# Kernel optimization log

Hardware: AMD Instinct MI355X
Metric: run time of the kernel (lower is better)

Reference implementation:

```python
import jax, jax.numpy as jnp
import numpy as np

N, E = 50000, 800000
NFEAT, NHID, NHEADS, NCLASS = 512, 64, 8, 64
ALPHA = 0.2  # leaky relu negative slope


def setup_inputs() -> dict:
    key = jax.random.key(0)
    ks = jax.random.split(key, 8)
    x = jax.random.normal(ks[0], (N, NFEAT), jnp.float32)
    row = jax.random.randint(ks[1], (E,), 0, N)  # destination node i of each edge
    col = jax.random.randint(ks[2], (E,), 0, N)  # source node j of each edge
    W = jax.random.normal(ks[3], (NHEADS, NFEAT, NHID), jnp.float32) * (1.0 / np.sqrt(NFEAT))
    a = jax.random.normal(ks[4], (NHEADS, 2 * NHID), jnp.float32) * 0.1
    W_out = jax.random.normal(ks[5], (NHID * NHEADS, NCLASS), jnp.float32) * (1.0 / np.sqrt(NHID * NHEADS))
    a_out = jax.random.normal(ks[6], (2 * NCLASS,), jnp.float32) * 0.1
    return {"x": x, "row": row, "col": col, "W": W, "a": a, "W_out": W_out, "a_out": a_out}


def _gat_layer(h, W, a, row, col, n, alpha, concat):
    # h: [N, F_in], W: [F_in, F'], a: [2*F']
    Wh = h @ W                                   # [N, F']
    f = Wh.shape[-1]
    f_dst = Wh @ a[:f]                           # a^T part for target node i, [N]
    f_src = Wh @ a[f:]                           # a^T part for source node j, [N]
    e = jax.nn.leaky_relu(f_dst[row] + f_src[col], alpha)       # [E] attention logits
    # numerically stable segment softmax over incoming edges of each node
    m = jax.ops.segment_max(e, row, num_segments=n)
    m = jnp.where(jnp.isneginf(m), 0.0, m)       # nodes with no in-edges
    p = jnp.exp(e - m[row])
    denom = jax.ops.segment_sum(p, row, num_segments=n)
    att = p / jnp.maximum(denom[row], 1e-16)     # [E]
    out = jax.ops.segment_sum(att[:, None] * Wh[col], row, num_segments=n)  # [N, F']
    return jax.nn.elu(out) if concat else out


def reference(x, row, col, W, a, W_out, a_out):
    # eval mode: F.dropout is a no-op
    heads = [_gat_layer(x, W[h], a[h], row, col, N, ALPHA, True) for h in range(NHEADS)]
    h = jnp.concatenate(heads, axis=1)           # [N, NHID*NHEADS]
    return _gat_layer(h, W_out, a_out, row, col, N, ALPHA, False)  # [N, NCLASS]
```

## Files before the change

kernel.cpp:

```cpp
#include <hip/hip_runtime.h>
#include <cstdint>
#include <cstddef>

#define NN      50000
#define MPAD    50048
#define EE      800000
#define NHEADS  8
#define HID_TOT 512
#define NCLASS  64
#define ALPHA_LRELU 0.2f
#define NB1     196

typedef unsigned short u16;
typedef __attribute__((ext_vector_type(8))) unsigned short ushort8;
typedef __attribute__((ext_vector_type(4))) unsigned short ushort4v;

__device__ __forceinline__ float bf2f(u16 v) {
    return __uint_as_float(((unsigned)v) << 16);
}
__device__ __forceinline__ u16 f2bf(float f) {
    unsigned u = __float_as_uint(f);
    return (u16)((u + 0x7fffu + ((u >> 16) & 1u)) >> 16);
}

#define PREP_R0 (MPAD * 64)
#define PREP_R1 (512 * 512)
#define PREP_R2 (64 * 512)
#define PREP_R3 (NN / 4)
#define PREP_TOT (PREP_R0 + PREP_R1 + PREP_R2 + PREP_R3)

__global__ __launch_bounds__(256) void prep_all(const float* __restrict__ x,
                                                const float* __restrict__ W,
                                                const float* __restrict__ W_out,
                                                u16* __restrict__ xb,
                                                u16* __restrict__ Wt1,
                                                u16* __restrict__ Wto,
                                                int* __restrict__ cnt) {
    int g = blockIdx.x * 256 + threadIdx.x;
    if (g < PREP_R0) {
        int r = g >> 6;
        int c = (g & 63) * 8;
        ushort8 o = (ushort8)0;
        if (r < NN) {
            const float4 v0 = *(const float4*)(x + (size_t)r * 512 + c);
            const float4 v1 = *(const float4*)(x + (size_t)r * 512 + c + 4);
            o[0] = f2bf(v0.x); o[1] = f2bf(v0.y); o[2] = f2bf(v0.z); o[3] = f2bf(v0.w);
            o[4] = f2bf(v1.x); o[5] = f2bf(v1.y); o[6] = f2bf(v1.z); o[7] = f2bf(v1.w);
        }
        *(ushort8*)(xb + (size_t)r * 512 + c) = o;
        return;
    }
    g -= PREP_R0;
    if (g < PREP_R1) {
        int c = g >> 9, f = g & 511;
        int h = c >> 6, j = c & 63;
        Wt1[g] = f2bf(W[(h << 15) + (f << 6) + j]);
        return;
    }
    g -= PREP_R1;
    if (g < PREP_R2) {
        int n = g >> 9, k = g & 511;
        Wto[g] = f2bf(W_out[k * 64 + n]);
        return;
    }
    g -= PREP_R2;
    if (g < PREP_R3) {
        *(int4*)(cnt + g * 4) = make_int4(0, 0, 0, 0);
    }
}


__global__ void hist_rows(const int* __restrict__ row, int* __restrict__ cnt) {
    int e = blockIdx.x * 256 + threadIdx.x;
    if (e >= EE) return;
    atomicAdd(&cnt[row[e]], 1);
}

__global__ __launch_bounds__(256) void scan_blocksum(const int* __restrict__ cnt,
                                                     int* __restrict__ bsum) {
    int idx = blockIdx.x * 256 + threadIdx.x;
    int v = (idx < NN) ? cnt[idx] : 0;
    #pragma unroll
    for (int o = 32; o; o >>= 1) v += __shfl_xor(v, o);
    __shared__ int sw[4];
    int wave = threadIdx.x >> 6;
    if ((threadIdx.x & 63) == 0) sw[wave] = v;
    __syncthreads();
    if (threadIdx.x == 0) bsum[blockIdx.x] = sw[0] + sw[1] + sw[2] + sw[3];
}

__global__ __launch_bounds__(256) void scan_bsums(const int* __restrict__ bsum,
                                                  int* __restrict__ boff) {
    __shared__ int sh[256];
    int t = threadIdx.x;
    int v = (t < NB1) ? bsum[t] : 0;
    sh[t] = v;
    __syncthreads();
    for (int o = 1; o < 256; o <<= 1) {
        int cur = sh[t];
        int add = (t >= o) ? sh[t - o] : 0;
        __syncthreads();
        sh[t] = cur + add;
        __syncthreads();
    }
    if (t < NB1) boff[t] = sh[t] - v;
}

__global__ __launch_bounds__(256) void scan_write(const int* __restrict__ cnt,
                                                  const int* __restrict__ boff,
                                                  int* __restrict__ start,
                                                  int* __restrict__ wr) {
    __shared__ int sh[256];
    int t = threadIdx.x;
    int idx = blockIdx.x * 256 + t;
    int c = (idx < NN) ? cnt[idx] : 0;
    sh[t] = c;
    __syncthreads();
    for (int o = 1; o < 256; o <<= 1) {
        int cur = sh[t];
        int add = (t >= o) ? sh[t - o] : 0;
        __syncthreads();
        sh[t] = cur + add;
        __syncthreads();
    }
    if (idx < NN) {
        int excl = boff[blockIdx.x] + sh[t] - c;
        start[idx] = excl;
        wr[idx] = excl;
    }
    if (idx == 0) start[NN] = EE;
}

__global__ void scatter_edges(const int* __restrict__ row, const int* __restrict__ col,
                              int* __restrict__ wr, int* __restrict__ ecol) {
    int e = blockIdx.x * 256 + threadIdx.x;
    if (e >= EE) return;
    int i = row[e];
    int pos = atomicAdd(&wr[i], 1);
    ecol[pos] = col[e];
}


__device__ __forceinline__ void load_lds_128(const u16* g, u16* l) {
    __builtin_amdgcn_global_load_lds((const __attribute__((address_space(1))) void*)g,
                                     (__attribute__((address_space(3))) void*)l,
                                     16, 0, 0);
}

typedef __attribute__((ext_vector_type(8))) short frag8;
typedef __attribute__((ext_vector_type(4))) float f32x4;

template <int BN, int OUT_MODE, int FUSE>
__global__ __launch_bounds__(256) void gemm_bf16(const u16* __restrict__ A,
                                                 const u16* __restrict__ Bt,
                                                 void* __restrict__ Cv,
                                                 int M, int N, int K,
                                                 const float* __restrict__ av,
                                                 float* __restrict__ fd,
                                                 float* __restrict__ fs) {
    constexpr int BM = 128, BK = 32;
    constexpr int WN = BN / 2;
    constexpr int NT = WN / 16;
    __shared__ u16 As[BM * BK];
    __shared__ u16 Bs[BN * BK];
    __shared__ float pd[2][2][64];
    __shared__ float ps[2][2][64];
    const int tid = threadIdx.x;
    const int wave = tid >> 6, lane = tid & 63;
    const int wm = wave & 1, wn = wave >> 1;
    const int bm = blockIdx.x * BM, bn = blockIdx.y * BN;
    const int q = lane >> 4, lr = lane & 15;

    f32x4 acc[4][NT] = {};

    for (int k0 = 0; k0 < K; k0 += BK) {
        #pragma unroll
        for (int c = wave; c < (BM * BK) / 512; c += 4) {
            int f = c * 512 + lane * 8;
            int row = f >> 5, ck = f & 31;
            load_lds_128(A + (size_t)(bm + row) * K + k0 + ck, As + c * 512);
        }
        #pragma unroll
        for (int c = wave; c < (BN * BK) / 512; c += 4) {
            int f = c * 512 + lane * 8;
            int row = f >> 5, ck = f & 31;
            load_lds_128(Bt + (size_t)(bn + row) * K + k0 + ck, Bs + c * 512);
        }
        __syncthreads();
        frag8 af[4], bfr[NT];
        #pragma unroll
        for (int am = 0; am < 4; am++)
            af[am] = *(const frag8*)(As + (wm * 64 + am * 16 + lr) * 32 + q * 8);
        #pragma unroll
        for (int bt = 0; bt < NT; bt++)
            bfr[bt] = *(const frag8*)(Bs + (wn * WN + bt * 16 + lr) * 32 + q * 8);
        #pragma unroll
        for (int am = 0; am < 4; am++)
            #pragma unroll
            for (int bt = 0; bt < NT; bt++)
                acc[am][bt] = __builtin_amdgcn_mfma_f32_16x16x32_bf16(af[am], bfr[bt], acc[am][bt], 0, 0, 0);
        __syncthreads();
    }

    float adv[NT], adv2[NT];
    int hd = 0;
    if (FUSE == 1) {
        hd = blockIdx.y * 2 + wn;
        const float* ah = av + hd * 128;
        #pragma unroll
        for (int bt = 0; bt < NT; bt++) {
            adv[bt]  = ah[bt * 16 + lr];
            adv2[bt] = ah[64 + bt * 16 + lr];
        }
    }
    if (FUSE == 2) {
        #pragma unroll
        for (int bt = 0; bt < NT; bt++) {
            adv[bt]  = av[wn * WN + bt * 16 + lr];
            adv2[bt] = av[64 + wn * WN + bt * 16 + lr];
        }
    }

    #pragma unroll
    for (int am = 0; am < 4; am++) {
        #pragma unroll
        for (int reg = 0; reg < 4; reg++) {
            int gr = bm + wm * 64 + am * 16 + q * 4 + reg;
            bool inb = gr < M;
            if (inb) {
                #pragma unroll
                for (int bt = 0; bt < NT; bt++) {
                    int gc = bn + wn * WN + bt * 16 + lr;
                    float v = acc[am][bt][reg];
                    if (OUT_MODE == 0) ((float*)Cv)[(size_t)gr * N + gc] = v;
                    else               ((u16*)Cv)[(size_t)gr * N + gc] = f2bf(v);
                }
            }
            if (FUSE != 0) {
                float sd = 0.f, ss = 0.f;
                #pragma unroll
                for (int bt = 0; bt < NT; bt++) {
                    float v = acc[am][bt][reg];
                    sd += v * adv[bt];
                    ss += v * adv2[bt];
                }
                #pragma unroll
                for (int o = 1; o < 16; o <<= 1) {
                    sd += __shfl_xor(sd, o);
                    ss += __shfl_xor(ss, o);
                }
                if (FUSE == 1) {
                    if (lr == 0 && inb) {
                        fd[gr * 8 + hd] = sd;
                        fs[gr * 8 + hd] = ss;
                    }
                } else {
                    if (lr == 0) {
                        int rr = am * 16 + q * 4 + reg;
                        pd[wm][wn][rr] = sd;
                        ps[wm][wn][rr] = ss;
                    }
                }
            }
        }
    }
    if (FUSE == 2) {
        __syncthreads();
        if (tid < 128) {
            int wmm = tid >> 6, rr = tid & 63;
            int gr = bm + wmm * 64 + rr;
            if (gr < M) {
                fd[gr] = pd[wmm][0][rr] + pd[wmm][1][rr];
                fs[gr] = ps[wmm][0][rr] + ps[wmm][1][rr];
            }
        }
    }
}

__global__ __launch_bounds__(256) void agg1_fused(const int* __restrict__ start,
                                                  const int* __restrict__ ecol,
                                                  const float* __restrict__ fd,
                                                  const float* __restrict__ fs,
                                                  const u16* __restrict__ Whb,
                                                  u16* __restrict__ h1b) {
    const int i = blockIdx.x * 4 + (threadIdx.x >> 6);
    const int lane = threadIdx.x & 63;
    const int hh = lane >> 3;
    const int st = start[i], en = start[i + 1];
    const float fdv = fd[i * 8 + hh];

    float acc[8] = {};
    float den = 0.f;
    int t = st;
    for (; t + 2 <= en; t += 2) {
        int j0 = ecol[t], j1 = ecol[t + 1];
        float v0 = fdv + fs[j0 * 8 + hh]; v0 = v0 > 0.f ? v0 : ALPHA_LRELU * v0;
        float v1 = fdv + fs[j1 * 8 + hh]; v1 = v1 > 0.f ? v1 : ALPHA_LRELU * v1;
        float p0 = __expf(v0);
        float p1 = __expf(v1);
        ushort8 w0 = *(const ushort8*)(Whb + (size_t)j0 * HID_TOT + lane * 8);
        ushort8 w1 = *(const ushort8*)(Whb + (size_t)j1 * HID_TOT + lane * 8);
        den += p0 + p1;
        #pragma unroll
        for (int k = 0; k < 8; k++) acc[k] += p0 * bf2f(w0[k]);
        #pragma unroll
        for (int k = 0; k < 8; k++) acc[k] += p1 * bf2f(w1[k]);
    }
    if (t < en) {
        int j = ecol[t];
        float v = fdv + fs[j * 8 + hh]; v = v > 0.f ? v : ALPHA_LRELU * v;
        float p = __expf(v);
        den += p;
        ushort8 wv = *(const ushort8*)(Whb + (size_t)j * HID_TOT + lane * 8);
        #pragma unroll
        for (int k = 0; k < 8; k++) acc[k] += p * bf2f(wv[k]);
    }
    float rden = 1.0f / fmaxf(den, 1e-16f);
    ushort8 o8;
    #pragma unroll
    for (int k = 0; k < 8; k++) {
        float v = acc[k] * rden;
        v = v > 0.f ? v : (__expf(v) - 1.0f);
        o8[k] = f2bf(v);
    }
    *(ushort8*)(h1b + (size_t)i * HID_TOT + lane * 8) = o8;
}

__global__ __launch_bounds__(256) void agg2_fused(const int* __restrict__ start,
                                                  const int* __restrict__ ecol,
                                                  const float* __restrict__ fd,
                                                  const float* __restrict__ fs,
                                                  const u16* __restrict__ Wh2b,
                                                  float* __restrict__ out) {
    const int i = blockIdx.x * 4 + (threadIdx.x >> 6);
    const int lane = threadIdx.x & 63;
    const int g = lane >> 4, r = lane & 15;
    const int st = start[i], en = start[i + 1];
    const float fdv = fd[i];

    float acc[4] = {};
    float den = 0.f;
    for (int t = st + g; t < en; t += 4) {
        int j = ecol[t];
        float v = fdv + fs[j];
        v = v > 0.f ? v : ALPHA_LRELU * v;
        float p = __expf(v);
        den += p;
        ushort4v wv = *(const ushort4v*)(Wh2b + (size_t)j * NCLASS + r * 4);
        #pragma unroll
        for (int k = 0; k < 4; k++) acc[k] += p * bf2f(wv[k]);
    }
    #pragma unroll
    for (int o = 16; o <= 32; o <<= 1) {
        den += __shfl_xor(den, o);
        #pragma unroll
        for (int k = 0; k < 4; k++) acc[k] += __shfl_xor(acc[k], o);
    }
    if (g == 0) {
        float rden = 1.0f / fmaxf(den, 1e-16f);
        float4 o4;
        o4.x = acc[0] * rden; o4.y = acc[1] * rden;
        o4.z = acc[2] * rden; o4.w = acc[3] * rden;
        *(float4*)(out + (size_t)i * NCLASS + r * 4) = o4;
    }
}


static inline int cdiv_l(long a, long b) { return (int)((a + b - 1) / b); }

extern "C" void kernel_launch(void* const* d_in, const int* in_sizes, int n_in,
                              void* d_out, int out_size, void* d_ws, size_t ws_size,
                              hipStream_t stream) {
    const float* x     = (const float*)d_in[0];
    const int*   row   = (const int*)d_in[1];
    const int*   col   = (const int*)d_in[2];
    const float* W     = (const float*)d_in[3];
    const float* a     = (const float*)d_in[4];
    const float* W_out = (const float*)d_in[5];
    const float* a_out = (const float*)d_in[6];
    float* out = (float*)d_out;

    char* wsb = (char*)d_ws;
    size_t off = 0;
    auto alloc = [&](size_t bytes) { char* p = wsb + off; off += (bytes + 255) & ~(size_t)255; return p; };
    u16*   xb     = (u16*)  alloc((size_t)MPAD * 512 * 2);
    u16*   Wcat_t = (u16*)  alloc((size_t)512 * 512 * 2);
    u16*   Wot_t  = (u16*)  alloc((size_t)64 * 512 * 2);
    u16*   Whb1   = (u16*)  alloc((size_t)NN * 512 * 2);
    float* fd1    = (float*)alloc((size_t)NN * 8 * 4);
    float* fs1    = (float*)alloc((size_t)NN * 8 * 4);
    u16*   h1b    = (u16*)  alloc((size_t)MPAD * 512 * 2);
    u16*   Wh2b   = (u16*)  alloc((size_t)NN * 64 * 2);
    float* fd2    = (float*)alloc((size_t)NN * 4);
    float* fs2    = (float*)alloc((size_t)NN * 4);
    int*   cnt    = (int*)  alloc((size_t)NN * 4);
    int*   startp = (int*)  alloc(((size_t)NN + 1) * 4);
    int*   wr     = (int*)  alloc((size_t)NN * 4);
    int*   ecol   = (int*)  alloc((size_t)EE * 4);
    int*   bsum   = (int*)  alloc((size_t)NB1 * 4);
    int*   boff   = (int*)  alloc((size_t)NB1 * 4);

    prep_all<<<cdiv_l(PREP_TOT, 256), 256, 0, stream>>>(x, W, W_out, xb, Wcat_t, Wot_t, cnt);

    hist_rows<<<cdiv_l(EE, 256), 256, 0, stream>>>(row, cnt);
    scan_blocksum<<<NB1, 256, 0, stream>>>(cnt, bsum);
    scan_bsums<<<1, 256, 0, stream>>>(bsum, boff);
    scan_write<<<NB1, 256, 0, stream>>>(cnt, boff, startp, wr);
    scatter_edges<<<cdiv_l(EE, 256), 256, 0, stream>>>(row, col, wr, ecol);

    {
        dim3 grid(cdiv_l(MPAD, 128), 512 / 128);
        gemm_bf16<128, 1, 1><<<grid, 256, 0, stream>>>(xb, Wcat_t, Whb1, NN, 512, 512,
                                                       a, fd1, fs1);
    }
    agg1_fused<<<NN / 4, 256, 0, stream>>>(startp, ecol, fd1, fs1, Whb1, h1b);

    {
        dim3 grid(cdiv_l(MPAD, 128), 1);
        gemm_bf16<64, 1, 2><<<grid, 256, 0, stream>>>(h1b, Wot_t, Wh2b, NN, 64, 512,
                                                      a_out, fd2, fs2);
    }
    agg2_fused<<<NN / 4, 256, 0, stream>>>(startp, ecol, fd2, fs2, Wh2b, out);
}
```

Measured before the change: 489.3 us.

## Merge CSR build kernels and co-schedule edge scatter with first GEMM

Folds the row histogram into the prep kernel, with the counter zeroing moved to a memset. The separate block-sum scan is removed by having each scan_write block sum its predecessor block totals itself. The edge scatter and the first-layer GEMM now run in one launch, with disjoint block ranges doing each job. This cuts several launches and lets the atomic-bound scatter overlap with the matrix work, at the cost of a specialised GEMM copy and redundant prefix summation per block.

```diff
diff --git a/kernel.cpp b/kernel.cpp
--- a/kernel.cpp
+++ b/kernel.cpp
@@ -10,6 +10,8 @@
 #define NCLASS  64
 #define ALPHA_LRELU 0.2f
 #define NB1     196
+#define NSCAT   3125
+#define GM1_M   391
 
 typedef unsigned short u16;
 typedef __attribute__((ext_vector_type(8))) unsigned short ushort8;
@@ -26,8 +28,7 @@
 #define PREP_R0 (MPAD * 64)
 #define PREP_R1 (512 * 512)
 #define PREP_R2 (64 * 512)
-#define PREP_R3 (NN / 4)
-#define PREP_TOT (PREP_R0 + PREP_R1 + PREP_R2 + PREP_R3)
+#define PREP_TOT (PREP_R0 + PREP_R1 + PREP_R2 + EE)
 
 __global__ __launch_bounds__(256) void prep_all(const float* __restrict__ x,
                                                 const float* __restrict__ W,
@@ -35,6 +36,7 @@
                                                 u16* __restrict__ xb,
                                                 u16* __restrict__ Wt1,
                                                 u16* __restrict__ Wto,
+                                                const int* __restrict__ row,
                                                 int* __restrict__ cnt) {
     int g = blockIdx.x * 256 + threadIdx.x;
     if (g < PREP_R0) {
@@ -64,17 +66,11 @@
         return;
     }
     g -= PREP_R2;
-    if (g < PREP_R3) {
-        *(int4*)(cnt + g * 4) = make_int4(0, 0, 0, 0);
-    }
-}
-
-
-__global__ void hist_rows(const int* __restrict__ row, int* __restrict__ cnt) {
-    int e = blockIdx.x * 256 + threadIdx.x;
-    if (e >= EE) return;
-    atomicAdd(&cnt[row[e]], 1);
-}
+    if (g < EE) {
+        atomicAdd(&cnt[row[g]], 1);
+    }
+}
+
 
 __global__ __launch_bounds__(256) void scan_blocksum(const int* __restrict__ cnt,
                                                      int* __restrict__ bsum) {
@@ -89,31 +85,23 @@
     if (threadIdx.x == 0) bsum[blockIdx.x] = sw[0] + sw[1] + sw[2] + sw[3];
 }
 
-__global__ __launch_bounds__(256) void scan_bsums(const int* __restrict__ bsum,
-                                                  int* __restrict__ boff) {
-    __shared__ int sh[256];
-    int t = threadIdx.x;
-    int v = (t < NB1) ? bsum[t] : 0;
-    sh[t] = v;
-    __syncthreads();
-    for (int o = 1; o < 256; o <<= 1) {
-        int cur = sh[t];
-        int add = (t >= o) ? sh[t - o] : 0;
-        __syncthreads();
-        sh[t] = cur + add;
-        __syncthreads();
-    }
-    if (t < NB1) boff[t] = sh[t] - v;
-}
-
 __global__ __launch_bounds__(256) void scan_write(const int* __restrict__ cnt,
-                                                  const int* __restrict__ boff,
+                                                  const int* __restrict__ bsum,
                                                   int* __restrict__ start,
                                                   int* __restrict__ wr) {
     __shared__ int sh[256];
+    __shared__ int swb[4];
     int t = threadIdx.x;
+    int vb = (t < NB1 && t < blockIdx.x) ? bsum[t] : 0;
+    #pragma unroll
+    for (int o = 32; o; o >>= 1) vb += __shfl_xor(vb, o);
+    if ((t & 63) == 0) swb[t >> 6] = vb;
+    __syncthreads();
+    const int blockoff = swb[0] + swb[1] + swb[2] + swb[3];
+
     int idx = blockIdx.x * 256 + t;
     int c = (idx < NN) ? cnt[idx] : 0;
+    __syncthreads();
     sh[t] = c;
     __syncthreads();
     for (int o = 1; o < 256; o <<= 1) {
@@ -124,20 +112,11 @@
         __syncthreads();
     }
     if (idx < NN) {
-        int excl = boff[blockIdx.x] + sh[t] - c;
+        int excl = blockoff + sh[t] - c;
         start[idx] = excl;
         wr[idx] = excl;
     }
     if (idx == 0) start[NN] = EE;
-}
-
-__global__ void scatter_edges(const int* __restrict__ row, const int* __restrict__ col,
-                              int* __restrict__ wr, int* __restrict__ ecol) {
-    int e = blockIdx.x * 256 + threadIdx.x;
-    if (e >= EE) return;
-    int i = row[e];
-    int pos = atomicAdd(&wr[i], 1);
-    ecol[pos] = col[e];
 }
 
 
@@ -149,6 +128,112 @@
 
 typedef __attribute__((ext_vector_type(8))) short frag8;
 typedef __attribute__((ext_vector_type(4))) float f32x4;
+
+__global__ __launch_bounds__(256) void scat_gemm1(const int* __restrict__ row,
+                                                  const int* __restrict__ col,
+                                                  int* __restrict__ wr,
+                                                  int* __restrict__ ecol,
+                                                  const u16* __restrict__ A,
+                                                  const u16* __restrict__ Bt,
+                                                  u16* __restrict__ C,
+                                                  const float* __restrict__ av,
+                                                  float* __restrict__ fd,
+                                                  float* __restrict__ fs) {
+    constexpr int BM = 128, BN = 128, BK = 32, WN = 64, NT = 4;
+    constexpr int M = NN, N = 512, K = 512;
+    __shared__ u16 As[BM * BK];
+    __shared__ u16 Bs[BN * BK];
+    const int tid = threadIdx.x;
+
+    if (blockIdx.x < NSCAT) {
+        int e = blockIdx.x * 256 + tid;
+        if (e < EE) {
+            int i = row[e];
+            int pos = atomicAdd(&wr[i], 1);
+            ecol[pos] = col[e];
+        }
+        return;
+    }
+    const int bid = blockIdx.x - NSCAT;
+    const int wave = tid >> 6, lane = tid & 63;
+    const int wm = wave & 1, wn = wave >> 1;
+    const int bm = (bid % GM1_M) * BM;
+    const int bnb = bid / GM1_M;
+    const int bn = bnb * BN;
+    const int q = lane >> 4, lr = lane & 15;
+
+    f32x4 acc[4][NT] = {};
+
+    for (int k0 = 0; k0 < K; k0 += BK) {
+        #pragma unroll
+        for (int c = wave; c < (BM * BK) / 512; c += 4) {
+            int f = c * 512 + lane * 8;
+            int r_ = f >> 5, ck = f & 31;
+            load_lds_128(A + (size_t)(bm + r_) * K + k0 + ck, As + c * 512);
+        }
+        #pragma unroll
+        for (int c = wave; c < (BN * BK) / 512; c += 4) {
+            int f = c * 512 + lane * 8;
+            int r_ = f >> 5, ck = f & 31;
+            load_lds_128(Bt + (size_t)(bn + r_) * K + k0 + ck, Bs + c * 512);
+        }
+        __syncthreads();
+        frag8 af[4], bfr[NT];
+        #pragma unroll
+        for (int am = 0; am < 4; am++)
+            af[am] = *(const frag8*)(As + (wm * 64 + am * 16 + lr) * 32 + q * 8);
+        #pragma unroll
+        for (int bt = 0; bt < NT; bt++)
+            bfr[bt] = *(const frag8*)(Bs + (wn * WN + bt * 16 + lr) * 32 + q * 8);
+        #pragma unroll
+        for (int am = 0; am < 4; am++)
+            #pragma unroll
+            for (int bt = 0; bt < NT; bt++)
+                acc[am][bt] = __builtin_amdgcn_mfma_f32_16x16x32_bf16(af[am], bfr[bt], acc[am][bt], 0, 0, 0);
+        __syncthreads();
+    }
+
+    const int hd = bnb * 2 + wn;
+    const float* ah = av + hd * 128;
+    float adv[NT], adv2[NT];
+    #pragma unroll
+    for (int bt = 0; bt < NT; bt++) {
+        adv[bt]  = ah[bt * 16 + lr];
+        adv2[bt] = ah[64 + bt * 16 + lr];
+    }
+
+    #pragma unroll
+    for (int am = 0; am < 4; am++) {
+        #pragma unroll
+        for (int reg = 0; reg < 4; reg++) {
+            int gr = bm + wm * 64 + am * 16 + q * 4 + reg;
+            bool inb = gr < M;
+            if (inb) {
+                #pragma unroll
+                for (int bt = 0; bt < NT; bt++) {
+                    int gc = bn + wn * WN + bt * 16 + lr;
+                    C[(size_t)gr * N + gc] = f2bf(acc[am][bt][reg]);
+                }
+            }
+            float sd = 0.f, ss = 0.f;
+            #pragma unroll
+            for (int bt = 0; bt < NT; bt++) {
+                float v = acc[am][bt][reg];
+                sd += v * adv[bt];
+                ss += v * adv2[bt];
+            }
+            #pragma unroll
+            for (int o = 1; o < 16; o <<= 1) {
+                sd += __shfl_xor(sd, o);
+                ss += __shfl_xor(ss, o);
+            }
+            if (lr == 0 && inb) {
+                fd[gr * 8 + hd] = sd;
+                fs[gr * 8 + hd] = ss;
+            }
+        }
+    }
+}
 
 template <int BN, int OUT_MODE, int FUSE>
 __global__ __launch_bounds__(256) void gemm_bf16(const u16* __restrict__ A,
@@ -399,20 +484,18 @@
     int*   ecol   = (int*)  alloc((size_t)EE * 4);
     int*   bsum   = (int*)  alloc((size_t)NB1 * 4);
     int*   boff   = (int*)  alloc((size_t)NB1 * 4);
-
-    prep_all<<<cdiv_l(PREP_TOT, 256), 256, 0, stream>>>(x, W, W_out, xb, Wcat_t, Wot_t, cnt);
-
-    hist_rows<<<cdiv_l(EE, 256), 256, 0, stream>>>(row, cnt);
+    (void)boff;
+
+    hipMemsetAsync(cnt, 0, (size_t)NN * 4, stream);
+    prep_all<<<cdiv_l(PREP_TOT, 256), 256, 0, stream>>>(x, W, W_out, xb, Wcat_t, Wot_t,
+                                                        row, cnt);
+
     scan_blocksum<<<NB1, 256, 0, stream>>>(cnt, bsum);
-    scan_bsums<<<1, 256, 0, stream>>>(bsum, boff);
-    scan_write<<<NB1, 256, 0, stream>>>(cnt, boff, startp, wr);
-    scatter_edges<<<cdiv_l(EE, 256), 256, 0, stream>>>(row, col, wr, ecol);
-
-    {
-        dim3 grid(cdiv_l(MPAD, 128), 512 / 128);
-        gemm_bf16<128, 1, 1><<<grid, 256, 0, stream>>>(xb, Wcat_t, Whb1, NN, 512, 512,
-                                                       a, fd1, fs1);
-    }
+    scan_write<<<NB1, 256, 0, stream>>>(cnt, bsum, startp, wr);
+
+    scat_gemm1<<<NSCAT + GM1_M * 4, 256, 0, stream>>>(row, col, wr, ecol,
+                                                      xb, Wcat_t, Whb1, a, fd1, fs1);
+
     agg1_fused<<<NN / 4, 256, 0, stream>>>(startp, ecol, fd1, fs1, Whb1, h1b);
 
     {
```

Result: no change. 487.8 us (-0.3%).
